# Kernel tuning notes

Hardware: AMD Instinct MI355X
Metric: run time of the kernel (lower is better)

Reference implementation:

```python
import jax, jax.numpy as jnp
import numpy as np

B, NA, NR, D, H, DH = 2, 4096, 512, 128, 8, 16
N_LOCAL, N_IPA, N_ITER = 5, 4, 3


def rots_from_vec(v):
    # quaternion (1, vx, vy, vz) normalized -> rotation matrix (AlphaFold-style update)
    q = jnp.concatenate([jnp.ones(v.shape[:-1] + (1,), v.dtype), v], axis=-1)
    q = q / jnp.linalg.norm(q, axis=-1, keepdims=True)
    w, x, y, z = q[..., 0], q[..., 1], q[..., 2], q[..., 3]
    R = jnp.stack([
        1 - 2 * (y * y + z * z), 2 * (x * y - w * z), 2 * (x * z + w * y),
        2 * (x * y + w * z), 1 - 2 * (x * x + z * z), 2 * (y * z - w * x),
        2 * (x * z - w * y), 2 * (y * z + w * x), 1 - 2 * (x * x + y * y)], axis=-1)
    return R.reshape(v.shape[:-1] + (3, 3))


def apply_frames(R, t, x):
    return jnp.einsum('...ij,...j->...i', R, x) + t


def invert_frames(R, t):
    Rt = jnp.swapaxes(R, -1, -2)
    return Rt, -jnp.einsum('...ij,...j->...i', Rt, t)


def pool_atoms_to_res(atom_feats, res_map):
    # scatter-mean: atoms -> residues
    d = atom_feats.shape[-1]
    idx = (res_map + jnp.arange(B, dtype=res_map.dtype)[:, None] * NR).reshape(-1)
    sums = jax.ops.segment_sum(atom_feats.reshape(-1, d), idx, num_segments=B * NR)
    cnts = jax.ops.segment_sum(jnp.ones((B * NA, 1), atom_feats.dtype), idx, num_segments=B * NR)
    return (sums / (cnts + 1e-8)).reshape(B, NR, d)


def setup_inputs() -> dict:
    key = jax.random.key(0)
    ks = iter(jax.random.split(key, 40))
    s = 0.02
    inp = dict(
        coords_bad=jax.random.normal(next(ks), (B, NA, 3), jnp.float32) * 5.0,
        atom_types=jax.random.randint(next(ks), (B, NA), 0, 20),
        residue_types=jax.random.randint(next(ks), (B, NA), 0, 21),
        mask=jnp.ones((B, NA), jnp.float32),
        res_mask=jnp.ones((B, NR), jnp.float32),
        res_map=jnp.sort(jax.random.randint(next(ks), (B, NA), 0, NR), axis=-1),
        rots_bad=rots_from_vec(0.1 * jax.random.normal(next(ks), (B, NR, 3), jnp.float32)),
        trans_bad=jax.random.normal(next(ks), (B, NR, 3), jnp.float32) * 5.0,
        atom_emb=jax.random.normal(next(ks), (20, D), jnp.float32) * s,
        res_emb=jax.random.normal(next(ks), (21, D), jnp.float32) * s,
        coord_W=jax.random.normal(next(ks), (3, D), jnp.float32) * s,
        coord_b=jnp.zeros((D,), jnp.float32),
        local_W=jax.random.normal(next(ks), (N_LOCAL, D, D), jnp.float32) * s,
        local_b=jnp.zeros((N_LOCAL, D), jnp.float32),
        pair_W=jax.random.normal(next(ks), (4, D), jnp.float32) * s,
        pair_b=jnp.zeros((D,), jnp.float32),
        ipa_Wq=jax.random.normal(next(ks), (N_IPA, D, H * DH), jnp.float32) * s,
        ipa_Wk=jax.random.normal(next(ks), (N_IPA, D, H * DH), jnp.float32) * s,
        ipa_Wv=jax.random.normal(next(ks), (N_IPA, D, H * DH), jnp.float32) * s,
        ipa_Wb=jax.random.normal(next(ks), (N_IPA, D, H), jnp.float32) * s,
        ipa_Wo=jax.random.normal(next(ks), (N_IPA, H * DH, D), jnp.float32) * s,
        ipa_bo=jnp.zeros((N_IPA, D), jnp.float32),
        head_W=jax.random.normal(next(ks), (D, 6), jnp.float32) * s,
        head_b=jnp.zeros((6,), jnp.float32),
    )
    return inp


def reference(coords_bad, atom_types, residue_types, mask, res_mask, res_map,
              rots_bad, trans_bad, atom_emb, res_emb, coord_W, coord_b,
              local_W, local_b, pair_W, pair_b,
              ipa_Wq, ipa_Wk, ipa_Wv, ipa_Wb, ipa_Wo, ipa_bo, head_W, head_b):
    cur_R, cur_t = rots_bad, trans_bad
    mask_j = (res_mask > 0)[:, None, None, :]  # [B,1,1,NR]
    # encoder output is iteration-invariant (coords_bad fixed), hoist it
    atom_feats = atom_emb[atom_types] + res_emb[residue_types] + coords_bad @ coord_W + coord_b
    feats0 = pool_atoms_to_res(atom_feats, res_map)  # [B,NR,D]
    for _ in range(N_ITER):
        feats = feats0
        residual = feats
        for l in range(N_LOCAL):
            feats = jax.nn.gelu(feats @ local_W[l] + local_b[l]) + residual
            residual = feats
        rel = cur_t[:, :, None, :] - cur_t[:, None, :, :]          # [B,NR,NR,3]
        dist = jnp.linalg.norm(rel, axis=-1, keepdims=True)
        pairwise = jnp.concatenate([rel, dist], axis=-1) @ pair_W + pair_b  # [B,NR,NR,D]
        for l in range(N_IPA):
            q = (feats @ ipa_Wq[l]).reshape(B, NR, H, DH)
            k = (feats @ ipa_Wk[l]).reshape(B, NR, H, DH)
            v = (feats @ ipa_Wv[l]).reshape(B, NR, H, DH)
            bias = jnp.transpose(pairwise @ ipa_Wb[l], (0, 3, 1, 2))  # [B,H,NR,NR]
            logits = jnp.einsum('bihd,bjhd->bhij', q, k) / np.float32(np.sqrt(DH)) + bias
            logits = jnp.where(mask_j, logits, jnp.float32(-1e9))
            attn = jax.nn.softmax(logits, axis=-1)
            o = jnp.einsum('bhij,bjhd->bihd', attn, v).reshape(B, NR, H * DH)
            feats = (o @ ipa_Wo[l] + ipa_bo[l]) + residual
            residual = feats
        upd = feats @ head_W + head_b                      # [B,NR,6]
        rot_vec, trans_vec = upd[..., :3], upd[..., 3:]
        cur_R = jnp.einsum('...ij,...jk->...ik', rots_from_vec(rot_vec), cur_R)
        cur_t = cur_t + jnp.einsum('...ij,...j->...i', cur_R, trans_vec)
        cur_t = cur_t * res_mask[..., None]
    inv_R, inv_t = invert_frames(rots_bad, trans_bad)
    bidx = jnp.arange(B)[:, None]
    local = apply_frames(inv_R[bidx, res_map], inv_t[bidx, res_map], coords_bad)
    final = apply_frames(jnp.swapaxes(cur_R[bidx, res_map], -1, -2), cur_t[bidx, res_map], local)
    return cur_R, cur_t, final
```

## Files before the change

### kernel.cpp

```cpp
#include <hip/hip_runtime.h>
#include <math.h>

#define B_ 2
#define NA_ 4096
#define NR_ 512
#define D_ 128
#define H_ 8
#define DH_ 16
#define NLOCAL_ 5
#define NIPA_ 4
#define NITER_ 3

typedef _Float16 half2_t __attribute__((ext_vector_type(2)));
typedef _Float16 f16x4 __attribute__((ext_vector_type(4)));
typedef float f32x4 __attribute__((ext_vector_type(4)));

#if __has_builtin(__builtin_amdgcn_fdot2)
#define FDOT2(a, b, c) __builtin_amdgcn_fdot2((a), (b), (c), false)
#else
__device__ __forceinline__ float FDOT2(half2_t a, half2_t b, float c) {
  return c + (float)a.x * (float)b.x + (float)a.y * (float)b.y;
}
#endif

#define MFMA16(a, b, c) __builtin_amdgcn_mfma_f32_16x16x16f16((a), (b), (c), 0, 0, 0)

__device__ __forceinline__ unsigned int pack_h(float a, float b) {
  union { unsigned int u; half2_t h; } x;
  x.h = half2_t{(_Float16)a, (_Float16)b};
  return x.u;
}
__device__ __forceinline__ half2_t u2h(unsigned int u) {
  union { unsigned int u; half2_t h; } x;
  x.u = u;
  return x.h;
}
__device__ __forceinline__ f16x4 mk4(unsigned int a, unsigned int b) {
  union { uint2 u; f16x4 h; } x;
  x.u = make_uint2(a, b);
  return x.h;
}
__device__ __forceinline__ float gelu_tanh(float x) {
  float x3 = x * x * x;
  return 0.5f * x * (1.0f + tanhf(0.7978845608028654f * (x + 0.044715f * x3)));
}

__device__ __forceinline__ void store_vT(unsigned int* vw, int h, int u, int rr,
                                         float b0, float b1) {
  unsigned int pk = pack_h(b0, b1);
  unsigned short* vt16 = (unsigned short*)vw;
  vt16[((h * 16 + 2 * u) << 10) + rr] = (unsigned short)(pk & 0xffffu);
  vt16[((h * 16 + 2 * u + 1) << 10) + rr] = (unsigned short)(pk >> 16);
}

__global__ __launch_bounds__(256) void k_setup(
    const float* __restrict__ coords, const int* __restrict__ atype,
    const int* __restrict__ rtype, const int* __restrict__ res_map,
    const float* __restrict__ rots_bad, const float* __restrict__ trans_bad,
    const float* __restrict__ res_mask,
    const float* __restrict__ atom_emb, const float* __restrict__ res_emb,
    const float* __restrict__ coord_W, const float* __restrict__ coord_b,
    const float* __restrict__ local_W, const float* __restrict__ pair_W,
    const float* __restrict__ pair_b, const float* __restrict__ Wq,
    const float* __restrict__ Wk, const float* __restrict__ Wv, const float* __restrict__ Wb,
    const float* __restrict__ Wo, float* __restrict__ feats0, float* __restrict__ weff,
    float* __restrict__ beff, float* __restrict__ curR, float* __restrict__ curT0,
    float4* __restrict__ ts4g0, unsigned int* __restrict__ lwh,
    unsigned int* __restrict__ qkvh, unsigned int* __restrict__ woh) {
  int tid = threadIdx.x, bid = blockIdx.x;
  int gtid = (bid << 8) + tid;
  for (int t = gtid; t < 172032; t += 65536) {
    if (t < 40960) {
      int c = t & 127, kk = (t >> 7) & 63, l = t >> 13;
      const float* s = local_W + (size_t)l * 16384 + (2 * kk) * 128 + c;
      lwh[t] = pack_h(s[0], s[128]);
    } else if (t < 139264) {
      int t2 = t - 40960;
      int c = t2 & 127, kk = (t2 >> 7) & 63, lm = t2 >> 13;
      int l = lm / 3, m = lm % 3;
      const float* base = (m == 0) ? Wq : ((m == 1) ? Wk : Wv);
      const float* s = base + (size_t)l * 16384 + (2 * kk) * 128 + c;
      qkvh[t2] = pack_h(s[0], s[128]);
    } else {
      int t3 = t - 139264;
      int c = t3 & 127, kk = (t3 >> 7) & 63, l = t3 >> 13;
      const float* s = Wo + (size_t)l * 16384 + (2 * kk) * 128 + c;
      woh[t3] = pack_h(s[0], s[128]);
    }
  }
  if (gtid < 160) {
    int l = gtid / 40, rest = gtid % 40;
    int c = rest / 8, h = rest & 7;
    const float* row = (c < 4) ? (pair_W + c * D_) : pair_b;
    float acc = 0.f;
    for (int d = 0; d < D_; d++) acc += row[d] * Wb[l * D_ * H_ + d * H_ + h];
    if (c < 4) weff[l * 32 + c * 8 + h] = acc;
    else beff[l * 8 + h] = acc;
  }
  if (gtid < 9216) curR[gtid] = rots_bad[gtid];
  else if (gtid < 12288) curT0[gtid - 9216] = trans_bad[gtid - 9216];
  if (gtid < 1024)
    ts4g0[gtid] = make_float4(trans_bad[gtid * 3], trans_bad[gtid * 3 + 1],
                              trans_bad[gtid * 3 + 2], res_mask[gtid]);
  for (int rp = 0; rp < 2; rp++) {
    int row = (bid << 2) + (rp << 1) + (tid >> 7);
    int d = tid & 127;
    int b = row >> 9, rr = row & (NR_ - 1);
    const int* rm = res_map + b * NA_;
    int lo = 0, hi = NA_;
    while (lo < hi) { int mid = (lo + hi) >> 1; if (rm[mid] < rr) lo = mid + 1; else hi = mid; }
    int start = lo;
    hi = NA_;
    while (lo < hi) { int mid = (lo + hi) >> 1; if (rm[mid] < rr + 1) lo = mid + 1; else hi = mid; }
    int end = lo;
    float w0 = coord_W[d], w1 = coord_W[D_ + d], w2 = coord_W[2 * D_ + d], cb = coord_b[d];
    float s = 0.f;
    for (int a = start; a < end; a++) {
      int ga = b * NA_ + a;
      s += atom_emb[atype[ga] * D_ + d] + res_emb[rtype[ga] * D_ + d] +
           coords[ga * 3 + 0] * w0 + coords[ga * 3 + 1] * w1 + coords[ga * 3 + 2] * w2 + cb;
    }
    feats0[row * D_ + d] = s / ((float)(end - start) + 1e-8f);
  }
}

__global__ __launch_bounds__(256) void k_localA(
    const float* __restrict__ feats0, const unsigned int* __restrict__ lwh,
    const float* __restrict__ local_b, const unsigned int* __restrict__ qkvh,
    float* __restrict__ featsL, unsigned int* __restrict__ qbU,
    unsigned int* __restrict__ kw, unsigned int* __restrict__ vw) {
  __shared__ unsigned int xh[4][64];
  __shared__ float xsf[4][128];
  int tid = threadIdx.x;
  int w = tid >> 6, cp = tid & 63;
  int row0 = blockIdx.x << 2;
  int row = row0 + w;
  float2 x2 = *(const float2*)(feats0 + (size_t)row * D_ + 2 * cp);
  float y0 = x2.x, y1 = x2.y;
  xsf[w][2 * cp] = y0; xsf[w][2 * cp + 1] = y1;
  xh[w][cp] = pack_h(y0, y1);
  for (int l = 0; l < NLOCAL_; l++) {
    const unsigned int* W = lwh + l * 8192;
    float a0 = 0.f, a1 = 0.f;
#pragma unroll 8
    for (int kk = 0; kk < 64; kk++) {
      uint2 ww = *(const uint2*)(W + kk * 128 + 2 * cp);
      half2_t x = u2h(xh[w][kk]);
      a0 = FDOT2(x, u2h(ww.x), a0);
      a1 = FDOT2(x, u2h(ww.y), a1);
    }
    y0 = gelu_tanh(a0 + local_b[l * D_ + 2 * cp]) + xsf[w][2 * cp];
    y1 = gelu_tanh(a1 + local_b[l * D_ + 2 * cp + 1]) + xsf[w][2 * cp + 1];
    xsf[w][2 * cp] = y0; xsf[w][2 * cp + 1] = y1;
    xh[w][cp] = pack_h(y0, y1);
  }
  *(float2*)(featsL + (size_t)row * D_ + 2 * cp) = make_float2(y0, y1);
  __syncthreads();
  if (w < 3) {
    const unsigned int* Wm = qkvh + (size_t)w * 8192;
    float bacc[4][2] = {};
#pragma unroll 8
    for (int kk = 0; kk < 64; kk++) {
      uint2 ww = *(const uint2*)(Wm + kk * 128 + 2 * cp);
#pragma unroll
      for (int r = 0; r < 4; r++) {
        half2_t x = u2h(xh[r][kk]);
        bacc[r][0] = FDOT2(x, u2h(ww.x), bacc[r][0]);
        bacc[r][1] = FDOT2(x, u2h(ww.y), bacc[r][1]);
      }
    }
    int h = cp >> 3, u = cp & 7;
#pragma unroll
    for (int r = 0; r < 4; r++) {
      int rr = row0 + r;
      if (w == 0) qbU[rr * 64 + cp] = pack_h(bacc[r][0], bacc[r][1]);
      else if (w == 1) kw[((h << 10) + rr) * 8 + u] = pack_h(bacc[r][0], bacc[r][1]);
      else store_vT(vw, h, u, rr, bacc[r][0], bacc[r][1]);
    }
  }
}

__global__ __launch_bounds__(256) void k_attn(
    const unsigned int* __restrict__ qbU, const unsigned int* __restrict__ kr,
    const unsigned int* __restrict__ vtg, const float4* __restrict__ ts4g,
    const float* __restrict__ weff, const float* __restrict__ beff,
    float* __restrict__ ob, int l) {
  __shared__ float osum[4][64][5];
  int tid = threadIdx.x, bid = blockIdx.x;
  int w = tid >> 6, lane = tid & 63;
  int qt = bid & 31, bh = bid >> 5;
  int b = bh >> 3, h = bh & 7;
  int lrow = lane & 15, lgrp = lane >> 4;
  int qrow = (b << 9) + qt * 16 + lrow;
  const uint2 qp = *(const uint2*)(qbU + (size_t)qrow * 64 + h * 8 + lgrp * 2);
  f16x4 qf = mk4(qp.x, qp.y);
  const float4* tb = ts4g + (b << 9);
  float4 ti = tb[qt * 16 + lrow];
  float c0 = weff[l * 32 + h], c1 = weff[l * 32 + 8 + h];
  float c2 = weff[l * 32 + 16 + h], c3 = weff[l * 32 + 24 + h];
  float be = beff[l * 8 + h];
  const unsigned int* kbase = kr + ((size_t)((h << 10) + (b << 9))) * 8;
  const unsigned int* vbase = vtg + (((h * 16 + lrow) << 9) + (b << 8));
  f32x4 zero = {0.f, 0.f, 0.f, 0.f};
  f32x4 oacc = zero;
  float lsum = 0.f;
#pragma unroll
  for (int jj = 0; jj < 8; jj++) {
    int jt = w * 8 + jj;
    int jr = jt * 16 + lrow;
    uint2 kp = *(const uint2*)(kbase + jr * 8 + lgrp * 2);
    f16x4 kf = mk4(kp.x, kp.y);
    f32x4 s = MFMA16(kf, qf, zero);
    f16x4 pv;
#pragma unroll
    for (int r = 0; r < 4; r++) {
      float4 tj = tb[jt * 16 + lgrp * 4 + r];
      float rx = ti.x - tj.x, ry = ti.y - tj.y, rz = ti.z - tj.z;
      float dist = sqrtf(rx * rx + ry * ry + rz * rz);
      float L = s[r] * 0.25f + c0 * rx + c1 * ry + c2 * rz + c3 * dist + be;
      L = (tj.w > 0.f) ? L : -1e9f;
      float p = __expf(L);
      lsum += p;
      pv[r] = (_Float16)p;
    }
    uint2 vp2 = *(const uint2*)(vbase + jt * 8 + lgrp * 2);
    f16x4 vf = mk4(vp2.x, vp2.y);
    oacc = MFMA16(vf, pv, oacc);
  }
  lsum += __shfl_xor(lsum, 16, 64);
  lsum += __shfl_xor(lsum, 32, 64);
  float* o = osum[w][lane];
  o[0] = oacc[0]; o[1] = oacc[1]; o[2] = oacc[2]; o[3] = oacc[3]; o[4] = lsum;
  __syncthreads();
  if (w == 0) {
    float s0 = 0.f, s1 = 0.f, s2 = 0.f, s3 = 0.f, sl = 0.f;
#pragma unroll
    for (int r = 0; r < 4; r++) {
      const float* p = osum[r][lane];
      s0 += p[0]; s1 += p[1]; s2 += p[2]; s3 += p[3]; sl += p[4];
    }
    float inv = 1.f / sl;
    float4 o4 = make_float4(s0 * inv, s1 * inv, s2 * inv, s3 * inv);
    *(float4*)(ob + (size_t)qrow * D_ + h * DH_ + lgrp * 4) = o4;
  }
}

__global__ __launch_bounds__(256) void k_oproj(
    const float* __restrict__ ob, const unsigned int* __restrict__ woh,
    const float* __restrict__ bo, const unsigned int* __restrict__ qkvh,
    const float* __restrict__ featsIn, float* __restrict__ featsW,
    const float* __restrict__ featsL, unsigned int* __restrict__ qbU,
    unsigned int* __restrict__ kw, unsigned int* __restrict__ vw,
    const float* __restrict__ curT_r, float* __restrict__ curT_w,
    float4* __restrict__ ts4g_w, float* __restrict__ curR,
    const float* __restrict__ res_mask, const float* __restrict__ head_W,
    const float* __restrict__ head_b, int l, int lastLayer, int doQ0) {
  __shared__ float part[4][2][128];
  __shared__ float xsf[2][128];
  __shared__ unsigned int xh[2][64];
  int tid = threadIdx.x;
  int w = tid >> 6, cp = tid & 63;
  int row0 = blockIdx.x << 1;
  if (w < 2) {
    float2 o2 = *(const float2*)(ob + (size_t)(row0 + w) * D_ + 2 * cp);
    xh[w][cp] = pack_h(o2.x, o2.y);
  }
  __syncthreads();
  {
    const unsigned int* W = woh + (size_t)l * 8192 + (w * 16) * 128;
    float a[2][2] = {};
#pragma unroll
    for (int kk = 0; kk < 16; kk++) {
      uint2 ww = *(const uint2*)(W + kk * 128 + 2 * cp);
#pragma unroll
      for (int r = 0; r < 2; r++) {
        half2_t x = u2h(xh[r][w * 16 + kk]);
        a[r][0] = FDOT2(x, u2h(ww.x), a[r][0]);
        a[r][1] = FDOT2(x, u2h(ww.y), a[r][1]);
      }
    }
#pragma unroll
    for (int r = 0; r < 2; r++) {
      part[w][r][2 * cp] = a[r][0];
      part[w][r][2 * cp + 1] = a[r][1];
    }
  }
  __syncthreads();
  {
    int r = tid >> 7, c = tid & 127;
    float f = part[0][r][c] + part[1][r][c] + part[2][r][c] + part[3][r][c] +
              bo[l * D_ + c] + featsIn[(size_t)(row0 + r) * D_ + c];
    featsW[(size_t)(row0 + r) * D_ + c] = f;
    xsf[r][c] = f;
  }
  __syncthreads();
  if (w < 2) xh[w][cp] = pack_h(xsf[w][2 * cp], xsf[w][2 * cp + 1]);
  __syncthreads();
  if (!lastLayer) {
    if (w < 3) {
      const unsigned int* Wm = qkvh + (size_t)((l + 1) * 3 + w) * 8192;
      float bacc[2][2] = {};
#pragma unroll 8
      for (int kk = 0; kk < 64; kk++) {
        uint2 ww = *(const uint2*)(Wm + kk * 128 + 2 * cp);
#pragma unroll
        for (int r = 0; r < 2; r++) {
          half2_t x = u2h(xh[r][kk]);
          bacc[r][0] = FDOT2(x, u2h(ww.x), bacc[r][0]);
          bacc[r][1] = FDOT2(x, u2h(ww.y), bacc[r][1]);
        }
      }
      int h = cp >> 3, u = cp & 7;
#pragma unroll
      for (int r = 0; r < 2; r++) {
        int rr = row0 + r;
        if (w == 0) qbU[rr * 64 + cp] = pack_h(bacc[r][0], bacc[r][1]);
        else if (w == 1) kw[((h << 10) + rr) * 8 + u] = pack_h(bacc[r][0], bacc[r][1]);
        else store_vT(vw, h, u, rr, bacc[r][0], bacc[r][1]);
      }
    }
  } else {
    if (w < 2) {
      int row = row0 + w;
      float f0 = xsf[w][2 * cp], f1 = xsf[w][2 * cp + 1];
      float pc[6];
#pragma unroll
      for (int c = 0; c < 6; c++)
        pc[c] = f0 * head_W[(2 * cp) * 6 + c] + f1 * head_W[(2 * cp + 1) * 6 + c];
#pragma unroll
      for (int m = 1; m < 64; m <<= 1)
#pragma unroll
        for (int c = 0; c < 6; c++) pc[c] += __shfl_xor(pc[c], m, 64);
      if (cp == 0) {
        float u[6];
#pragma unroll
        for (int c = 0; c < 6; c++) u[c] = pc[c] + head_b[c];
        float vx = u[0], vy = u[1], vz = u[2];
        float inv = rsqrtf(1.f + vx * vx + vy * vy + vz * vz);
        float qw = inv, qx = vx * inv, qy = vy * inv, qz = vz * inv;
        float Rd[9];
        Rd[0] = 1.f - 2.f * (qy * qy + qz * qz); Rd[1] = 2.f * (qx * qy - qw * qz);
        Rd[2] = 2.f * (qx * qz + qw * qy); Rd[3] = 2.f * (qx * qy + qw * qz);
        Rd[4] = 1.f - 2.f * (qx * qx + qz * qz); Rd[5] = 2.f * (qy * qz - qw * qx);
        Rd[6] = 2.f * (qx * qz - qw * qy); Rd[7] = 2.f * (qy * qz + qw * qx);
        Rd[8] = 1.f - 2.f * (qx * qx + qy * qy);
        float Ro[9];
#pragma unroll
        for (int c = 0; c < 9; c++) Ro[c] = curR[row * 9 + c];
        float Rn[9];
#pragma unroll
        for (int i2 = 0; i2 < 3; i2++)
#pragma unroll
          for (int kk = 0; kk < 3; kk++)
            Rn[i2 * 3 + kk] = Rd[i2 * 3 + 0] * Ro[0 * 3 + kk] +
                              Rd[i2 * 3 + 1] * Ro[1 * 3 + kk] +
                              Rd[i2 * 3 + 2] * Ro[2 * 3 + kk];
        float tx = curT_r[row * 3 + 0], ty = curT_r[row * 3 + 1], tz = curT_r[row * 3 + 2];
        float ux = u[3], uy = u[4], uz = u[5];
        float m = res_mask[row];
#pragma unroll
        for (int c = 0; c < 9; c++) curR[row * 9 + c] = Rn[c];
        float ntx = (tx + Rn[0] * ux + Rn[1] * uy + Rn[2] * uz) * m;
        float nty = (ty + Rn[3] * ux + Rn[4] * uy + Rn[5] * uz) * m;
        float ntz = (tz + Rn[6] * ux + Rn[7] * uy + Rn[8] * uz) * m;
        curT_w[row * 3 + 0] = ntx;
        curT_w[row * 3 + 1] = nty;
        curT_w[row * 3 + 2] = ntz;
        ts4g_w[row] = make_float4(ntx, nty, ntz, m);
      }
    }
    if (doQ0) {
      if (w < 2) {
        float2 fl = *(const float2*)(featsL + (size_t)(row0 + w) * D_ + 2 * cp);
        xh[w][cp] = pack_h(fl.x, fl.y);
      }
      __syncthreads();
      if (w < 3) {
        const unsigned int* Wm = qkvh + (size_t)w * 8192;
        float bacc[2][2] = {};
#pragma unroll 8
        for (int kk = 0; kk < 64; kk++) {
          uint2 ww = *(const uint2*)(Wm + kk * 128 + 2 * cp);
#pragma unroll
          for (int r = 0; r < 2; r++) {
            half2_t x = u2h(xh[r][kk]);
            bacc[r][0] = FDOT2(x, u2h(ww.x), bacc[r][0]);
            bacc[r][1] = FDOT2(x, u2h(ww.y), bacc[r][1]);
          }
        }
        int h = cp >> 3, u = cp & 7;
#pragma unroll
        for (int r = 0; r < 2; r++) {
          int rr = row0 + r;
          if (w == 0) qbU[rr * 64 + cp] = pack_h(bacc[r][0], bacc[r][1]);
          else if (w == 1) kw[((h << 10) + rr) * 8 + u] = pack_h(bacc[r][0], bacc[r][1]);
          else store_vT(vw, h, u, rr, bacc[r][0], bacc[r][1]);
        }
      }
    }
  }
}

__global__ void k_final(const float* __restrict__ coords, const int* __restrict__ res_map,
                        const float* __restrict__ rots_bad, const float* __restrict__ trans_bad,
                        const float* __restrict__ curR, const float* __restrict__ curT,
                        float* __restrict__ out) {
  int a = blockIdx.x * blockDim.x + threadIdx.x;
  if (a < B_ * NR_) {
#pragma unroll
    for (int c = 0; c < 9; c++) out[a * 9 + c] = curR[a * 9 + c];
    out[B_ * NR_ * 9 + a * 3 + 0] = curT[a * 3 + 0];
    out[B_ * NR_ * 9 + a * 3 + 1] = curT[a * 3 + 1];
    out[B_ * NR_ * 9 + a * 3 + 2] = curT[a * 3 + 2];
  }
  if (a >= B_ * NA_) return;
  int b = a / NA_;
  int r = b * NR_ + res_map[a];
  float x0 = coords[a * 3 + 0], x1 = coords[a * 3 + 1], x2 = coords[a * 3 + 2];
  float R0[9], Rc[9];
#pragma unroll
  for (int c = 0; c < 9; c++) { R0[c] = rots_bad[r * 9 + c]; Rc[c] = curR[r * 9 + c]; }
  float t0x = trans_bad[r * 3 + 0], t0y = trans_bad[r * 3 + 1], t0z = trans_bad[r * 3 + 2];
  float dx = x0 - t0x, dy = x1 - t0y, dz = x2 - t0z;
  float lx = R0[0] * dx + R0[3] * dy + R0[6] * dz;
  float ly = R0[1] * dx + R0[4] * dy + R0[7] * dz;
  float lz = R0[2] * dx + R0[5] * dy + R0[8] * dz;
  float tcx = curT[r * 3 + 0], tcy = curT[r * 3 + 1], tcz = curT[r * 3 + 2];
  float fx = Rc[0] * lx + Rc[3] * ly + Rc[6] * lz + tcx;
  float fy = Rc[1] * lx + Rc[4] * ly + Rc[7] * lz + tcy;
  float fz = Rc[2] * lx + Rc[5] * ly + Rc[8] * lz + tcz;
  int off = B_ * NR_ * 12;
  out[off + a * 3 + 0] = fx;
  out[off + a * 3 + 1] = fy;
  out[off + a * 3 + 2] = fz;
}

extern "C" void kernel_launch(void* const* d_in, const int* in_sizes, int n_in,
                              void* d_out, int out_size, void* d_ws, size_t ws_size,
                              hipStream_t stream) {
  const float* coords    = (const float*)d_in[0];
  const int*   atype     = (const int*)d_in[1];
  const int*   rtype     = (const int*)d_in[2];
  const float* res_mask  = (const float*)d_in[4];
  const int*   res_map   = (const int*)d_in[5];
  const float* rots_bad  = (const float*)d_in[6];
  const float* trans_bad = (const float*)d_in[7];
  const float* atom_emb  = (const float*)d_in[8];
  const float* res_emb   = (const float*)d_in[9];
  const float* coord_W   = (const float*)d_in[10];
  const float* coord_b   = (const float*)d_in[11];
  const float* local_W   = (const float*)d_in[12];
  const float* local_b   = (const float*)d_in[13];
  const float* pair_W    = (const float*)d_in[14];
  const float* pair_b    = (const float*)d_in[15];
  const float* Wq        = (const float*)d_in[16];
  const float* Wk        = (const float*)d_in[17];
  const float* Wv        = (const float*)d_in[18];
  const float* Wb        = (const float*)d_in[19];
  const float* Wo        = (const float*)d_in[20];
  const float* bo        = (const float*)d_in[21];
  const float* head_W    = (const float*)d_in[22];
  const float* head_b    = (const float*)d_in[23];

  float* ws = (float*)d_ws;
  float* ob     = ws;  ws += 131072;
  float* feats0 = ob;
  float* featsL = ws;  ws += 131072;
  float* featsW = ws;  ws += 131072;
  float* weff   = ws;  ws += 128;
  float* beff   = ws;  ws += 32;
  float* curR   = ws;  ws += 9216;
  float* curT0  = ws;  ws += 3072;
  float* curT1  = ws;  ws += 3072;
  float4* ts4g0 = (float4*)ws;  ws += 4096;
  float4* ts4g1 = (float4*)ws;  ws += 4096;
  unsigned int* wu = (unsigned int*)ws;
  unsigned int* qbU = wu;  wu += 65536;
  unsigned int* kbA = wu;  wu += 65536;
  unsigned int* vtA = wu;  wu += 65536;
  unsigned int* kbB = wu;  wu += 65536;
  unsigned int* vtB = wu;  wu += 65536;
  unsigned int* lwh  = wu; wu += 40960;
  unsigned int* qkvh = wu; wu += 98304;
  unsigned int* woh  = wu; wu += 32768;
  float* out = (float*)d_out;

  k_setup<<<256, 256, 0, stream>>>(coords, atype, rtype, res_map, rots_bad, trans_bad,
                                   res_mask, atom_emb, res_emb, coord_W, coord_b, local_W,
                                   pair_W, pair_b, Wq, Wk, Wv, Wb, Wo, feats0, weff, beff,
                                   curR, curT0, ts4g0, lwh, qkvh, woh);
  k_localA<<<256, 256, 0, stream>>>(feats0, lwh, local_b, qkvh, featsL, qbU, kbA, vtA);

  for (int iter = 0; iter < NITER_; iter++) {
    float* Tr = (iter & 1) ? curT1 : curT0;
    float* Tw = (iter & 1) ? curT0 : curT1;
    float4* Gr = (iter & 1) ? ts4g1 : ts4g0;
    float4* Gw = (iter & 1) ? ts4g0 : ts4g1;
    for (int l = 0; l < NIPA_; l++) {
      unsigned int* krd = (l & 1) ? kbB : kbA;
      unsigned int* vrd = (l & 1) ? vtB : vtA;
      unsigned int* kwr = (l & 1) ? kbA : kbB;
      unsigned int* vwr = (l & 1) ? vtA : vtB;
      k_attn<<<512, 256, 0, stream>>>(qbU, krd, vrd, Gr, weff, beff, ob, l);
      k_oproj<<<512, 256, 0, stream>>>(ob, woh, bo, qkvh, (l == 0) ? featsL : featsW,
                                       featsW, featsL, qbU, kwr, vwr, Tr, Tw, Gw, curR,
                                       res_mask, head_W, head_b, l,
                                       (l == NIPA_ - 1) ? 1 : 0,
                                       (l == NIPA_ - 1 && iter < NITER_ - 1) ? 1 : 0);
    }
  }
  k_final<<<(B_ * NA_ + 255) / 256, 256, 0, stream>>>(coords, res_map, rots_bad, trans_bad,
                                                      curR, curT1, out);
}
```

Measured before the change: 233.7 us.

## Fuse IPA attention and output projection into a single per-layer kernel

Merges the attention kernel and the output/QKV projection kernel into one k_layer kernel. Each 512-thread block owns 16 query rows across all 8 heads, so the intermediate attention output stays in shared memory and the ob global buffer and one launch per layer are gone. The block also precomputes pairwise displacement and distance terms once into shared memory as fp16, and evaluates the geometric bias with fdot2 instead of per-element fp32 math. In exchange the grid shrinks from 512 to 64 blocks, and each wave runs a 4x longer key loop, which risks underusing the GPU.

Result: slower. 379.3 us (+62.3%).

```diff
diff --git a/kernel.cpp b/kernel.cpp
--- a/kernel.cpp
+++ b/kernel.cpp
@@ -180,149 +180,145 @@
   }
 }
 
-__global__ __launch_bounds__(256) void k_attn(
-    const unsigned int* __restrict__ qbU, const unsigned int* __restrict__ kr,
-    const unsigned int* __restrict__ vtg, const float4* __restrict__ ts4g,
+__global__ __launch_bounds__(512) void k_layer(
+    unsigned int* __restrict__ qbU, const unsigned int* __restrict__ kr,
+    const unsigned int* __restrict__ vtg, unsigned int* __restrict__ kw,
+    unsigned int* __restrict__ vw, const float4* __restrict__ ts4g,
     const float* __restrict__ weff, const float* __restrict__ beff,
-    float* __restrict__ ob, int l) {
-  __shared__ float osum[4][64][5];
-  int tid = threadIdx.x, bid = blockIdx.x;
-  int w = tid >> 6, lane = tid & 63;
-  int qt = bid & 31, bh = bid >> 5;
-  int b = bh >> 3, h = bh & 7;
-  int lrow = lane & 15, lgrp = lane >> 4;
-  int qrow = (b << 9) + qt * 16 + lrow;
-  const uint2 qp = *(const uint2*)(qbU + (size_t)qrow * 64 + h * 8 + lgrp * 2);
-  f16x4 qf = mk4(qp.x, qp.y);
-  const float4* tb = ts4g + (b << 9);
-  float4 ti = tb[qt * 16 + lrow];
-  float c0 = weff[l * 32 + h], c1 = weff[l * 32 + 8 + h];
-  float c2 = weff[l * 32 + 16 + h], c3 = weff[l * 32 + 24 + h];
-  float be = beff[l * 8 + h];
-  const unsigned int* kbase = kr + ((size_t)((h << 10) + (b << 9))) * 8;
-  const unsigned int* vbase = vtg + (((h * 16 + lrow) << 9) + (b << 8));
-  f32x4 zero = {0.f, 0.f, 0.f, 0.f};
-  f32x4 oacc = zero;
-  float lsum = 0.f;
-#pragma unroll
-  for (int jj = 0; jj < 8; jj++) {
-    int jt = w * 8 + jj;
-    int jr = jt * 16 + lrow;
-    uint2 kp = *(const uint2*)(kbase + jr * 8 + lgrp * 2);
-    f16x4 kf = mk4(kp.x, kp.y);
-    f32x4 s = MFMA16(kf, qf, zero);
-    f16x4 pv;
-#pragma unroll
-    for (int r = 0; r < 4; r++) {
-      float4 tj = tb[jt * 16 + lgrp * 4 + r];
-      float rx = ti.x - tj.x, ry = ti.y - tj.y, rz = ti.z - tj.z;
-      float dist = sqrtf(rx * rx + ry * ry + rz * rz);
-      float L = s[r] * 0.25f + c0 * rx + c1 * ry + c2 * rz + c3 * dist + be;
-      L = (tj.w > 0.f) ? L : -1e9f;
-      float p = __expf(L);
-      lsum += p;
-      pv[r] = (_Float16)p;
-    }
-    uint2 vp2 = *(const uint2*)(vbase + jt * 8 + lgrp * 2);
-    f16x4 vf = mk4(vp2.x, vp2.y);
-    oacc = MFMA16(vf, pv, oacc);
-  }
-  lsum += __shfl_xor(lsum, 16, 64);
-  lsum += __shfl_xor(lsum, 32, 64);
-  float* o = osum[w][lane];
-  o[0] = oacc[0]; o[1] = oacc[1]; o[2] = oacc[2]; o[3] = oacc[3]; o[4] = lsum;
-  __syncthreads();
-  if (w == 0) {
-    float s0 = 0.f, s1 = 0.f, s2 = 0.f, s3 = 0.f, sl = 0.f;
-#pragma unroll
-    for (int r = 0; r < 4; r++) {
-      const float* p = osum[r][lane];
-      s0 += p[0]; s1 += p[1]; s2 += p[2]; s3 += p[3]; sl += p[4];
-    }
-    float inv = 1.f / sl;
-    float4 o4 = make_float4(s0 * inv, s1 * inv, s2 * inv, s3 * inv);
-    *(float4*)(ob + (size_t)qrow * D_ + h * DH_ + lgrp * 4) = o4;
-  }
-}
-
-__global__ __launch_bounds__(256) void k_oproj(
-    const float* __restrict__ ob, const unsigned int* __restrict__ woh,
-    const float* __restrict__ bo, const unsigned int* __restrict__ qkvh,
-    const float* __restrict__ featsIn, float* __restrict__ featsW,
-    const float* __restrict__ featsL, unsigned int* __restrict__ qbU,
-    unsigned int* __restrict__ kw, unsigned int* __restrict__ vw,
+    const unsigned int* __restrict__ woh, const unsigned int* __restrict__ qkvh,
+    const float* __restrict__ bo, const float* __restrict__ featsIn,
+    float* __restrict__ featsW, const float* __restrict__ featsL,
     const float* __restrict__ curT_r, float* __restrict__ curT_w,
     float4* __restrict__ ts4g_w, float* __restrict__ curR,
     const float* __restrict__ res_mask, const float* __restrict__ head_W,
     const float* __restrict__ head_b, int l, int lastLayer, int doQ0) {
-  __shared__ float part[4][2][128];
-  __shared__ float xsf[2][128];
-  __shared__ unsigned int xh[2][64];
-  int tid = threadIdx.x;
-  int w = tid >> 6, cp = tid & 63;
-  int row0 = blockIdx.x << 1;
-  if (w < 2) {
-    float2 o2 = *(const float2*)(ob + (size_t)(row0 + w) * D_ + 2 * cp);
-    xh[w][cp] = pack_h(o2.x, o2.y);
+  __shared__ uint2 rel4[16][513];
+  __shared__ float msk[NR_];
+  __shared__ float osf[16][129];
+  __shared__ float xsf[16][128];
+  __shared__ unsigned int xh[16][64];
+  int tid = threadIdx.x, bid = blockIdx.x;
+  int b = bid >> 5, qt = bid & 31;
+  int row0 = (b << 9) + qt * 16;
+
+  {
+    float4 tj4 = ts4g[(b << 9) + tid];
+    msk[tid] = tj4.w;
+#pragma unroll
+    for (int e = 0; e < 16; e++) {
+      float4 tq = ts4g[row0 + e];
+      float rx = tq.x - tj4.x, ry = tq.y - tj4.y, rz = tq.z - tj4.z;
+      float dist = sqrtf(rx * rx + ry * ry + rz * rz);
+      rel4[e][tid] = make_uint2(pack_h(rx, ry), pack_h(rz, dist));
+    }
   }
   __syncthreads();
+
+  int w = tid >> 6, lane = tid & 63;
+  int h = w;
+  int lrow = lane & 15, lgrp = lane >> 4;
   {
-    const unsigned int* W = woh + (size_t)l * 8192 + (w * 16) * 128;
+    int qrow = row0 + lrow;
+    const uint2 qp = *(const uint2*)(qbU + (size_t)qrow * 64 + h * 8 + lgrp * 2);
+    f16x4 qf = mk4(qp.x, qp.y);
+    float c0 = weff[l * 32 + h], c1 = weff[l * 32 + 8 + h];
+    float c2 = weff[l * 32 + 16 + h], c3 = weff[l * 32 + 24 + h];
+    float be = beff[l * 8 + h];
+    half2_t wh0{(_Float16)c0, (_Float16)c1};
+    half2_t wh1{(_Float16)c2, (_Float16)c3};
+    const unsigned int* kbase = kr + ((size_t)((h << 10) + (b << 9))) * 8;
+    const unsigned int* vbase = vtg + (((h * 16 + lrow) << 9) + (b << 8));
+    f32x4 zero = {0.f, 0.f, 0.f, 0.f};
+    f32x4 oacc = zero;
+    float lsum = 0.f;
+#pragma unroll 4
+    for (int jt = 0; jt < 32; jt++) {
+      int jr = jt * 16 + lrow;
+      uint2 kp = *(const uint2*)(kbase + jr * 8 + lgrp * 2);
+      f16x4 kf = mk4(kp.x, kp.y);
+      f32x4 s = MFMA16(kf, qf, zero);
+      f16x4 pv;
+#pragma unroll
+      for (int r = 0; r < 4; r++) {
+        int j = jt * 16 + lgrp * 4 + r;
+        uint2 rv = rel4[lrow][j];
+        float dot = FDOT2(u2h(rv.y), wh1, FDOT2(u2h(rv.x), wh0, 0.f));
+        float L = s[r] * 0.25f + dot + be;
+        L = (msk[j] > 0.f) ? L : -1e9f;
+        float p = __expf(L);
+        lsum += p;
+        pv[r] = (_Float16)p;
+      }
+      uint2 vp2 = *(const uint2*)(vbase + jt * 8 + lgrp * 2);
+      f16x4 vf = mk4(vp2.x, vp2.y);
+      oacc = MFMA16(vf, pv, oacc);
+    }
+    lsum += __shfl_xor(lsum, 16, 64);
+    lsum += __shfl_xor(lsum, 32, 64);
+    float inv = 1.f / lsum;
+#pragma unroll
+    for (int r = 0; r < 4; r++) osf[lrow][h * 16 + lgrp * 4 + r] = oacc[r] * inv;
+  }
+  __syncthreads();
+
+  int cp = lane;
+  int r0 = 2 * w, r1 = 2 * w + 1;
+  xh[r0][cp] = pack_h(osf[r0][2 * cp], osf[r0][2 * cp + 1]);
+  xh[r1][cp] = pack_h(osf[r1][2 * cp], osf[r1][2 * cp + 1]);
+  {
+    const unsigned int* W = woh + (size_t)l * 8192;
     float a[2][2] = {};
-#pragma unroll
-    for (int kk = 0; kk < 16; kk++) {
+#pragma unroll 8
+    for (int kk = 0; kk < 64; kk++) {
       uint2 ww = *(const uint2*)(W + kk * 128 + 2 * cp);
-#pragma unroll
-      for (int r = 0; r < 2; r++) {
-        half2_t x = u2h(xh[r][w * 16 + kk]);
-        a[r][0] = FDOT2(x, u2h(ww.x), a[r][0]);
-        a[r][1] = FDOT2(x, u2h(ww.y), a[r][1]);
-      }
+      half2_t x0 = u2h(xh[r0][kk]);
+      half2_t x1 = u2h(xh[r1][kk]);
+      a[0][0] = FDOT2(x0, u2h(ww.x), a[0][0]);
+      a[0][1] = FDOT2(x0, u2h(ww.y), a[0][1]);
+      a[1][0] = FDOT2(x1, u2h(ww.x), a[1][0]);
+      a[1][1] = FDOT2(x1, u2h(ww.y), a[1][1]);
     }
 #pragma unroll
     for (int r = 0; r < 2; r++) {
-      part[w][r][2 * cp] = a[r][0];
-      part[w][r][2 * cp + 1] = a[r][1];
-    }
-  }
-  __syncthreads();
-  {
-    int r = tid >> 7, c = tid & 127;
-    float f = part[0][r][c] + part[1][r][c] + part[2][r][c] + part[3][r][c] +
-              bo[l * D_ + c] + featsIn[(size_t)(row0 + r) * D_ + c];
-    featsW[(size_t)(row0 + r) * D_ + c] = f;
-    xsf[r][c] = f;
-  }
-  __syncthreads();
-  if (w < 2) xh[w][cp] = pack_h(xsf[w][2 * cp], xsf[w][2 * cp + 1]);
-  __syncthreads();
+      int rl = r0 + r;
+      int row = row0 + rl;
+      float f0 = a[r][0] + bo[l * D_ + 2 * cp] + featsIn[(size_t)row * D_ + 2 * cp];
+      float f1 = a[r][1] + bo[l * D_ + 2 * cp + 1] + featsIn[(size_t)row * D_ + 2 * cp + 1];
+      *(float2*)(featsW + (size_t)row * D_ + 2 * cp) = make_float2(f0, f1);
+      xsf[rl][2 * cp] = f0; xsf[rl][2 * cp + 1] = f1;
+      xh[rl][cp] = pack_h(f0, f1);
+    }
+  }
   if (!lastLayer) {
-    if (w < 3) {
-      const unsigned int* Wm = qkvh + (size_t)((l + 1) * 3 + w) * 8192;
+#pragma unroll
+    for (int m = 0; m < 3; m++) {
+      const unsigned int* Wm = qkvh + (size_t)((l + 1) * 3 + m) * 8192;
       float bacc[2][2] = {};
 #pragma unroll 8
       for (int kk = 0; kk < 64; kk++) {
         uint2 ww = *(const uint2*)(Wm + kk * 128 + 2 * cp);
-#pragma unroll
-        for (int r = 0; r < 2; r++) {
-          half2_t x = u2h(xh[r][kk]);
-          bacc[r][0] = FDOT2(x, u2h(ww.x), bacc[r][0]);
-          bacc[r][1] = FDOT2(x, u2h(ww.y), bacc[r][1]);
-        }
-      }
-      int h = cp >> 3, u = cp & 7;
+        half2_t x0 = u2h(xh[r0][kk]);
+        half2_t x1 = u2h(xh[r1][kk]);
+        bacc[0][0] = FDOT2(x0, u2h(ww.x), bacc[0][0]);
+        bacc[0][1] = FDOT2(x0, u2h(ww.y), bacc[0][1]);
+        bacc[1][0] = FDOT2(x1, u2h(ww.x), bacc[1][0]);
+        bacc[1][1] = FDOT2(x1, u2h(ww.y), bacc[1][1]);
+      }
+      int hh = cp >> 3, u = cp & 7;
 #pragma unroll
       for (int r = 0; r < 2; r++) {
-        int rr = row0 + r;
-        if (w == 0) qbU[rr * 64 + cp] = pack_h(bacc[r][0], bacc[r][1]);
-        else if (w == 1) kw[((h << 10) + rr) * 8 + u] = pack_h(bacc[r][0], bacc[r][1]);
-        else store_vT(vw, h, u, rr, bacc[r][0], bacc[r][1]);
+        int rr = row0 + r0 + r;
+        if (m == 0) qbU[rr * 64 + cp] = pack_h(bacc[r][0], bacc[r][1]);
+        else if (m == 1) kw[((hh << 10) + rr) * 8 + u] = pack_h(bacc[r][0], bacc[r][1]);
+        else store_vT(vw, hh, u, rr, bacc[r][0], bacc[r][1]);
       }
     }
   } else {
-    if (w < 2) {
-      int row = row0 + w;
-      float f0 = xsf[w][2 * cp], f1 = xsf[w][2 * cp + 1];
+#pragma unroll
+    for (int r = 0; r < 2; r++) {
+      int rl = r0 + r;
+      int row = row0 + rl;
+      float f0 = xsf[rl][2 * cp], f1 = xsf[rl][2 * cp + 1];
       float pc[6];
 #pragma unroll
       for (int c = 0; c < 6; c++)
@@ -370,31 +366,33 @@
       }
     }
     if (doQ0) {
-      if (w < 2) {
-        float2 fl = *(const float2*)(featsL + (size_t)(row0 + w) * D_ + 2 * cp);
-        xh[w][cp] = pack_h(fl.x, fl.y);
-      }
-      __syncthreads();
-      if (w < 3) {
-        const unsigned int* Wm = qkvh + (size_t)w * 8192;
+      {
+        float2 fl0 = *(const float2*)(featsL + (size_t)(row0 + r0) * D_ + 2 * cp);
+        float2 fl1 = *(const float2*)(featsL + (size_t)(row0 + r1) * D_ + 2 * cp);
+        xh[r0][cp] = pack_h(fl0.x, fl0.y);
+        xh[r1][cp] = pack_h(fl1.x, fl1.y);
+      }
+#pragma unroll
+      for (int m = 0; m < 3; m++) {
+        const unsigned int* Wm = qkvh + (size_t)m * 8192;
         float bacc[2][2] = {};
 #pragma unroll 8
         for (int kk = 0; kk < 64; kk++) {
           uint2 ww = *(const uint2*)(Wm + kk * 128 + 2 * cp);
-#pragma unroll
-          for (int r = 0; r < 2; r++) {
-            half2_t x = u2h(xh[r][kk]);
-            bacc[r][0] = FDOT2(x, u2h(ww.x), bacc[r][0]);
-            bacc[r][1] = FDOT2(x, u2h(ww.y), bacc[r][1]);
-          }
+          half2_t x0 = u2h(xh[r0][kk]);
+          half2_t x1 = u2h(xh[r1][kk]);
+          bacc[0][0] = FDOT2(x0, u2h(ww.x), bacc[0][0]);
+          bacc[0][1] = FDOT2(x0, u2h(ww.y), bacc[0][1]);
+          bacc[1][0] = FDOT2(x1, u2h(ww.x), bacc[1][0]);
+          bacc[1][1] = FDOT2(x1, u2h(ww.y), bacc[1][1]);
         }
-        int h = cp >> 3, u = cp & 7;
+        int hh = cp >> 3, u = cp & 7;
 #pragma unroll
         for (int r = 0; r < 2; r++) {
-          int rr = row0 + r;
-          if (w == 0) qbU[rr * 64 + cp] = pack_h(bacc[r][0], bacc[r][1]);
-          else if (w == 1) kw[((h << 10) + rr) * 8 + u] = pack_h(bacc[r][0], bacc[r][1]);
-          else store_vT(vw, h, u, rr, bacc[r][0], bacc[r][1]);
+          int rr = row0 + r0 + r;
+          if (m == 0) qbU[rr * 64 + cp] = pack_h(bacc[r][0], bacc[r][1]);
+          else if (m == 1) kw[((hh << 10) + rr) * 8 + u] = pack_h(bacc[r][0], bacc[r][1]);
+          else store_vT(vw, hh, u, rr, bacc[r][0], bacc[r][1]);
         }
       }
     }
@@ -463,8 +461,7 @@
   const float* head_b    = (const float*)d_in[23];
 
   float* ws = (float*)d_ws;
-  float* ob     = ws;  ws += 131072;
-  float* feats0 = ob;
+  float* feats0 = ws;  ws += 131072;
   float* featsL = ws;  ws += 131072;
   float* featsW = ws;  ws += 131072;
   float* weff   = ws;  ws += 128;
@@ -501,12 +498,11 @@
       unsigned int* vrd = (l & 1) ? vtB : vtA;
       unsigned int* kwr = (l & 1) ? kbA : kbB;
       unsigned int* vwr = (l & 1) ? vtA : vtB;
-      k_attn<<<512, 256, 0, stream>>>(qbU, krd, vrd, Gr, weff, beff, ob, l);
-      k_oproj<<<512, 256, 0, stream>>>(ob, woh, bo, qkvh, (l == 0) ? featsL : featsW,
-                                       featsW, featsL, qbU, kwr, vwr, Tr, Tw, Gw, curR,
-                                       res_mask, head_W, head_b, l,
-                                       (l == NIPA_ - 1) ? 1 : 0,
-                                       (l == NIPA_ - 1 && iter < NITER_ - 1) ? 1 : 0);
+      k_layer<<<64, 512, 0, stream>>>(qbU, krd, vrd, kwr, vwr, Gr, weff, beff, woh, qkvh,
+                                      bo, (l == 0) ? featsL : featsW, featsW, featsL,
+                                      Tr, Tw, Gw, curR, res_mask, head_W, head_b, l,
+                                      (l == NIPA_ - 1) ? 1 : 0,
+                                      (l == NIPA_ - 1 && iter < NITER_ - 1) ? 1 : 0);
     }
   }
   k_final<<<(B_ * NA_ + 255) / 256, 256, 0, stream>>>(coords, res_map, rots_bad, trans_bad,
```
